# Optimization experiments

Measured on AMD Instinct MI355X. Metric: run time of the kernel, lower is better.

The kernel has to match this reference:

```python
import jax, jax.numpy as jnp
import numpy as np

B, D, O, K = 8192, 256, 256, 16


def setup_inputs() -> dict:
    key = jax.random.key(0)
    k1, k2, k3, k4 = jax.random.split(key, 4)
    x = jax.random.normal(k1, (B, D), dtype=jnp.float32)
    # learned params
    values = jax.random.uniform(k2, (O, D, K), dtype=jnp.float32, minval=-0.05, maxval=0.05)
    skip_w = jax.random.normal(k3, (O, D), dtype=jnp.float32) * (1.0 / np.sqrt(D))
    skip_b = jax.random.uniform(k4, (O,), dtype=jnp.float32, minval=-1.0, maxval=1.0) / np.sqrt(D)
    # fixed buffer (non-trainable)
    grid = jnp.linspace(-1.0, 1.0, K).astype(jnp.float32)
    return {"x": x, "values": values, "skip_w": skip_w, "skip_b": skip_b, "grid": grid}


def reference(x, values, skip_w, skip_b, grid):
    # x: [B, D]; values: [O, D, K]; grid: [K]
    num_knots = grid.shape[0]
    xc = jnp.clip(x, -1.0, 1.0)
    # torch.bucketize(x, grid) (right=False) == searchsorted side='left'
    right = jnp.searchsorted(grid, xc, side="left")            # [B, D]
    left = jnp.clip(right - 1, 0, num_knots - 2)               # [B, D]
    right = left + 1
    g0 = grid[left]
    g1 = grid[right]
    w = (xc - g0) / (g1 - g0 + 1e-12)                          # [B, D]
    # sparse linear-interp coefficients over knots: 2 nonzeros per (b, d)
    coeff = (1.0 - w)[..., None] * jax.nn.one_hot(left, num_knots, dtype=xc.dtype) \
          + w[..., None] * jax.nn.one_hot(right, num_knots, dtype=xc.dtype)  # [B, D, K]
    # y[b,o] = sum_d sum_k coeff[b,d,k] * values[o,d,k]  (== per-dim gather+interp+accumulate)
    y = jnp.einsum("bdk,odk->bo", coeff, values)
    y = y + xc @ skip_w.T + skip_b
    return y
```

## Files before the change

### kernel.cpp

```cpp
#include <hip/hip_runtime.h>
#include <hip/hip_bf16.h>
#include <stdint.h>


#define D_DIM  256
#define O_DIM  256
#define BM     128
#define BK     64
#define KS     4
#define ITERS  16
#define NTHR   512

typedef __attribute__((ext_vector_type(8))) short bf16x8;
typedef __attribute__((ext_vector_type(4))) float f32x4;

__global__ __launch_bounds__(256) void kan_prep(
    const float* __restrict__ values,
    const float* __restrict__ skip_w,
    const float* __restrict__ gknots,
    const float* __restrict__ x,
    unsigned short* __restrict__ Vp)
{
    int tid = blockIdx.x * blockDim.x + threadIdx.x;
    int e = tid * 8;
    int o = e >> 12;
    int kflat = e & 4095;
    float sw = skip_w[(o << 8) | (kflat >> 4)];
    int kmod = kflat & 15;

    const float4* vp4 = reinterpret_cast<const float4*>(values + e);
    float4 v0 = vp4[0], v1 = vp4[1];
    float f[8] = {v0.x, v0.y, v0.z, v0.w, v1.x, v1.y, v1.z, v1.w};
    unsigned int w[4];
#pragma unroll
    for (int j = 0; j < 4; ++j) {
        float2 ab;
        ab.x = f[2*j]     + gknots[kmod + 2*j]     * sw;
        ab.y = f[2*j + 1] + gknots[kmod + 2*j + 1] * sw;
        __hip_bfloat162 p2 = __float22bfloat162_rn(ab);
        __builtin_memcpy(&w[j], &p2, 4);
    }
    size_t c = (size_t)(kflat >> 3) * 256 + (size_t)o;
    *reinterpret_cast<uint4*>(Vp + c * 8) = make_uint4(w[0], w[1], w[2], w[3]);

    {
        int pb = (int)blockIdx.x;
        int mt = (pb & 7) + 8 * ((pb >> 3) & 7);
        int rowbase = mt * BM + (pb >> 6) * 16;
        int t = (int)threadIdx.x;
        const float4* xw = reinterpret_cast<const float4*>(
            x + (size_t)(rowbase + (t >> 4)) * D_DIM) + (t & 15) * 4;
        float s = 0.f;
#pragma unroll
        for (int k = 0; k < 4; ++k) {
            float4 v = xw[k];
            s += v.x + v.y + v.z + v.w;
        }
        asm volatile("" :: "v"(s));
    }
}

__global__ __launch_bounds__(NTHR, 2) void kan_gemm(
    const float* __restrict__ x,
    const unsigned short* __restrict__ Vp,
    float* __restrict__ part,
    float* __restrict__ out)
{
    __shared__ unsigned short As[2][BM * BK];

    const int t    = threadIdx.x;
    const int lane = t & 63;
    const int wid  = t >> 6;
    const int wm   = wid >> 2;
    const int wn   = wid & 3;
    const int l15  = lane & 15;
    const int lhi  = lane >> 4;

    const int bid = (int)blockIdx.x;
    const int m8  = bid & 7;
    const int ks  = (bid >> 3) & 3;
    const int mhi = bid >> 5;
    const int mt  = m8 + 8 * mhi;
    const int bm0 = mt * BM;
    const size_t kc0 = (size_t)ks * 128;

    const int ar = t >> 2;
    const int ad = t & 3;
    const float* xp = x + (size_t)(bm0 + ar) * D_DIM + ks * 64 + ad;

    char* arow[2] = { (char*)&As[0][0] + ar * 128, (char*)&As[1][0] + ar * 128 };
    const int ca = ((2 * ad)     ^ (ar & 7)) * 16;
    const int cb = ((2 * ad + 1) ^ (ar & 7)) * 16;

    auto stageA = [&](int buf, float xv) {
        float xc = fminf(1.f, fmaxf(-1.f, xv));
        float tt = (xc + 1.f) * 7.5f;
        int li = (int)tt;
        li = li > 14 ? 14 : li;
        float w1 = tt - (float)li;
        float2 cw; cw.x = 1.f - w1; cw.y = w1;
        __hip_bfloat162 p2 = __float22bfloat162_rn(cw);
        unsigned int pk;
        __builtin_memcpy(&pk, &p2, 4);
        unsigned long long w64 = (unsigned long long)pk << ((li & 1) * 16);
        unsigned int lo = (unsigned int)w64;
        unsigned int hi = (unsigned int)(w64 >> 32);
        int jl = li >> 1;
        unsigned int wd[8];
#pragma unroll
        for (int j = 0; j < 8; ++j)
            wd[j] = (j == jl) ? lo : ((j == jl + 1) ? hi : 0u);
        char* a = arow[buf];
        *reinterpret_cast<uint4*>(a + ca) = make_uint4(wd[0], wd[1], wd[2], wd[3]);
        *reinterpret_cast<uint4*>(a + cb) = make_uint4(wd[4], wd[5], wd[6], wd[7]);
    };

    #define LOADB(BG, KT)                                                      \
        {                                                                      \
            const unsigned short* _b =                                         \
                Vp + (kc0 + (size_t)(KT) * 8) * 2048;                          \
            _Pragma("unroll")                                                  \
            for (int kh = 0; kh < 2; ++kh)                                     \
                _Pragma("unroll")                                              \
                for (int ni = 0; ni < 4; ++ni) {                               \
                    int n = wn * 64 + ni * 16 + l15;                           \
                    BG[kh * 4 + ni] = *reinterpret_cast<const bf16x8*>(        \
                        _b + ((size_t)((kh * 4 + lhi) * 256 + n)) * 8);        \
                }                                                              \
        }

    f32x4 acc[4][4] = {};
    bf16x8 bgA[8], bgB[8], bgC[8];

    int abyte[4], a7[4];
#pragma unroll
    for (int mi = 0; mi < 4; ++mi) {
        int m = wm * 64 + mi * 16 + l15;
        abyte[mi] = m * 128;
        a7[mi] = m & 7;
    }

    float xnxt = xp[0];
    LOADB(bgA, 0)
    LOADB(bgB, 1)
    stageA(0, xnxt);
    xnxt = xp[4];
    asm volatile("s_waitcnt lgkmcnt(0)" ::: "memory");
    __builtin_amdgcn_s_barrier();
    __builtin_amdgcn_sched_barrier(0);

    #define IT(KT, CUR, BGC_, BGN2)                                            \
        {                                                                      \
            const bool last = (KT) == ITERS - 1;                               \
            if ((KT) + 2 < ITERS) { LOADB(BGN2, (KT) + 2) }                    \
            const char* Ab = (const char*)&As[CUR][0];                         \
            bf16x8 af[4];                                                      \
                                                                   \
            _Pragma("unroll")                                                  \
            for (int mi = 0; mi < 4; ++mi)                                     \
                af[mi] = *reinterpret_cast<const bf16x8*>(                     \
                    Ab + abyte[mi] + ((lhi ^ a7[mi]) << 4));                   \
            __builtin_amdgcn_s_setprio(1);                                     \
            _Pragma("unroll")                                                  \
            for (int mi = 0; mi < 4; ++mi)                                     \
                _Pragma("unroll")                                              \
                for (int ni = 0; ni < 4; ++ni)                                 \
                    acc[mi][ni] = __builtin_amdgcn_mfma_f32_16x16x32_bf16(     \
                        af[mi], BGC_[ni], acc[mi][ni], 0, 0, 0);               \
            __builtin_amdgcn_s_setprio(0);                                     \
                                      \
            if (!last) {                                                       \
                stageA((CUR) ^ 1, xnxt);                                       \
                if ((KT) + 2 < ITERS) xnxt = xp[((KT) + 2) * 4];               \
            }                                                                  \
                                                                   \
            _Pragma("unroll")                                                  \
            for (int mi = 0; mi < 4; ++mi)                                     \
                af[mi] = *reinterpret_cast<const bf16x8*>(                     \
                    Ab + abyte[mi] + (((4 + lhi) ^ a7[mi]) << 4));             \
            __builtin_amdgcn_s_setprio(1);                                     \
            _Pragma("unroll")                                                  \
            for (int mi = 0; mi < 4; ++mi)                                     \
                _Pragma("unroll")                                              \
                for (int ni = 0; ni < 4; ++ni)                                 \
                    acc[mi][ni] = __builtin_amdgcn_mfma_f32_16x16x32_bf16(     \
                        af[mi], BGC_[4 + ni], acc[mi][ni], 0, 0, 0);           \
            __builtin_amdgcn_s_setprio(0);                                     \
            if (!last) {                                                       \
                asm volatile("s_waitcnt lgkmcnt(0)" ::: "memory");             \
                __builtin_amdgcn_s_barrier();                                  \
                __builtin_amdgcn_sched_barrier(0);                             \
            }                                                                  \
        }

    IT(0, 0, bgA, bgC)  IT(1, 1, bgB, bgA)  IT(2, 0, bgC, bgB)
    IT(3, 1, bgA, bgC)  IT(4, 0, bgB, bgA)  IT(5, 1, bgC, bgB)
    IT(6, 0, bgA, bgC)  IT(7, 1, bgB, bgA)  IT(8, 0, bgC, bgB)
    IT(9, 1, bgA, bgC)  IT(10, 0, bgB, bgA) IT(11, 1, bgC, bgB)
    IT(12, 0, bgA, bgC) IT(13, 1, bgB, bgA) IT(14, 0, bgC, bgB)
    IT(15, 1, bgA, bgC)
    #undef IT
    #undef LOADB

    float* dst = (ks == 0) ? out : part + (size_t)(ks - 1) * (8192 * 256);
#pragma unroll
    for (int ni = 0; ni < 4; ++ni) {
        int col = wn * 64 + ni * 16 + l15;
#pragma unroll
        for (int mi = 0; mi < 4; ++mi) {
            f32x4 v = acc[mi][ni];
            int row0 = bm0 + wm * 64 + mi * 16 + lhi * 4;
#pragma unroll
            for (int r = 0; r < 4; ++r)
                dst[(size_t)(row0 + r) * O_DIM + col] = v[r];
        }
    }
}

__global__ __launch_bounds__(256) void kan_reduce(
    const float* __restrict__ part,
    const float* __restrict__ skip_b,
    float* __restrict__ out)
{
    int rbid = (int)blockIdx.x;
    int c    = rbid & 7;
    int tq   = rbid >> 3;
    int mhi  = tq >> 5;
    int sub  = tq & 31;
    int mt   = c + 8 * mhi;
    int row0 = mt * BM + sub * 4;

    int i   = (int)threadIdx.x;
    int row = row0 + (i >> 6);
    int col = (i & 63) * 4;
    size_t e = (size_t)row * O_DIM + col;

    f32x4 s = *reinterpret_cast<const f32x4*>(out + e);
    s += *reinterpret_cast<const f32x4*>(skip_b + col);
    s += *reinterpret_cast<const f32x4*>(part + e);
    s += *reinterpret_cast<const f32x4*>(part + (size_t)8192 * 256 + e);
    s += *reinterpret_cast<const f32x4*>(part + (size_t)2 * 8192 * 256 + e);
    *reinterpret_cast<f32x4*>(out + e) = s;
}

__global__ __launch_bounds__(256) void kan_naive(
    const float* __restrict__ x,
    const unsigned short* __restrict__ Vp,
    const float* __restrict__ skip_b,
    float* __restrict__ out)
{
    int b = blockIdx.x, o = threadIdx.x;
    float acc = skip_b[o];
    for (int d = 0; d < 256; ++d) {
        float xc = fminf(1.f, fmaxf(-1.f, x[(size_t)b * 256 + d]));
        float tt = (xc + 1.f) * 7.5f;
        int li = (int)tt; li = li > 14 ? 14 : li;
        float w1 = tt - (float)li;
        int k0 = d * 16 + li;
        unsigned short u0 = Vp[((size_t)(k0 >> 3) * 256 + o) * 8 + (k0 & 7)];
        int k1 = k0 + 1;
        unsigned short u1 = Vp[((size_t)(k1 >> 3) * 256 + o) * 8 + (k1 & 7)];
        float f0 = __uint_as_float((unsigned)u0 << 16);
        float f1 = __uint_as_float((unsigned)u1 << 16);
        acc += (1.f - w1) * f0 + w1 * f1;
    }
    out[(size_t)b * 256 + o] = acc;
}

extern "C" void kernel_launch(void* const* d_in, const int* in_sizes, int n_in,
                              void* d_out, int out_size, void* d_ws, size_t ws_size,
                              hipStream_t stream) {
    const float* x      = (const float*)d_in[0];
    const float* values = (const float*)d_in[1];
    const float* skip_w = (const float*)d_in[2];
    const float* skip_b = (const float*)d_in[3];
    const float* gknots = (const float*)d_in[4];
    float* out = (float*)d_out;
    (void)in_sizes; (void)n_in; (void)out_size;

    unsigned short* Vp = (unsigned short*)d_ws;
    float* part = (float*)((char*)d_ws + 2u * 1024 * 1024);

    kan_prep<<<dim3(512), dim3(256), 0, stream>>>(values, skip_w, gknots, x, Vp);

    const size_t need = 2u * 1024 * 1024
                      + (size_t)3 * 8192 * 256 * sizeof(float);
    if (ws_size >= need) {
        kan_gemm<<<dim3(256), dim3(NTHR), 0, stream>>>(x, Vp, part, out);
        kan_reduce<<<dim3(2048), dim3(256), 0, stream>>>(part, skip_b, out);
    } else {
        kan_naive<<<dim3(8192), dim3(256), 0, stream>>>(x, Vp, skip_b, out);
    }
}
```

Measured before the change: 40.27 us.

## Give each wave private A tiles to eliminate block barriers in KAN GEMM

Halves the M tile to 64 rows with 256 threads and doubles the grid. Each wave now stages its own copy of the interpolation-coefficient A tile in LDS from float4 x loads, so the per-iteration workgroup barrier can be dropped. The cost is redundant coefficient computation and LDS writes across the four waves, plus more blocks and reloads of the B tiles.

```diff
diff --git a/kernel.cpp b/kernel.cpp
--- a/kernel.cpp
+++ b/kernel.cpp
@@ -5,11 +5,11 @@
 
 #define D_DIM  256
 #define O_DIM  256
-#define BM     128
+#define BM     64
 #define BK     64
 #define KS     4
 #define ITERS  16
-#define NTHR   512
+#define NTHR   256
 
 typedef __attribute__((ext_vector_type(8))) short bf16x8;
 typedef __attribute__((ext_vector_type(4))) float f32x4;
@@ -45,8 +45,8 @@
 
     {
         int pb = (int)blockIdx.x;
-        int mt = (pb & 7) + 8 * ((pb >> 3) & 7);
-        int rowbase = mt * BM + (pb >> 6) * 16;
+        int mt = (pb & 7) + 8 * ((pb >> 3) & 15);
+        int rowbase = mt * BM + (pb >> 7) * 16;
         int t = (int)threadIdx.x;
         const float4* xw = reinterpret_cast<const float4*>(
             x + (size_t)(rowbase + (t >> 4)) * D_DIM) + (t & 15) * 4;
@@ -66,13 +66,11 @@
     float* __restrict__ part,
     float* __restrict__ out)
 {
-    __shared__ unsigned short As[2][BM * BK];
+    __shared__ unsigned short As[4][2][64 * 64];
 
     const int t    = threadIdx.x;
     const int lane = t & 63;
     const int wid  = t >> 6;
-    const int wm   = wid >> 2;
-    const int wn   = wid & 3;
     const int l15  = lane & 15;
     const int lhi  = lane >> 4;
 
@@ -84,35 +82,39 @@
     const int bm0 = mt * BM;
     const size_t kc0 = (size_t)ks * 128;
 
-    const int ar = t >> 2;
-    const int ad = t & 3;
-    const float* xp = x + (size_t)(bm0 + ar) * D_DIM + ks * 64 + ad;
-
-    char* arow[2] = { (char*)&As[0][0] + ar * 128, (char*)&As[1][0] + ar * 128 };
-    const int ca = ((2 * ad)     ^ (ar & 7)) * 16;
-    const int cb = ((2 * ad + 1) ^ (ar & 7)) * 16;
-
-    auto stageA = [&](int buf, float xv) {
-        float xc = fminf(1.f, fmaxf(-1.f, xv));
-        float tt = (xc + 1.f) * 7.5f;
-        int li = (int)tt;
-        li = li > 14 ? 14 : li;
-        float w1 = tt - (float)li;
-        float2 cw; cw.x = 1.f - w1; cw.y = w1;
-        __hip_bfloat162 p2 = __float22bfloat162_rn(cw);
-        unsigned int pk;
-        __builtin_memcpy(&pk, &p2, 4);
-        unsigned long long w64 = (unsigned long long)pk << ((li & 1) * 16);
-        unsigned int lo = (unsigned int)w64;
-        unsigned int hi = (unsigned int)(w64 >> 32);
-        int jl = li >> 1;
-        unsigned int wd[8];
-#pragma unroll
-        for (int j = 0; j < 8; ++j)
-            wd[j] = (j == jl) ? lo : ((j == jl + 1) ? hi : 0u);
-        char* a = arow[buf];
-        *reinterpret_cast<uint4*>(a + ca) = make_uint4(wd[0], wd[1], wd[2], wd[3]);
-        *reinterpret_cast<uint4*>(a + cb) = make_uint4(wd[4], wd[5], wd[6], wd[7]);
+    const float* xr = x + (size_t)(bm0 + lane) * D_DIM + ks * 64;
+
+    char* abase[2] = { (char*)&As[wid][0][0] + lane * 128,
+                       (char*)&As[wid][1][0] + lane * 128 };
+    const int lsw = lane & 7;
+
+    auto stageA = [&](int buf, float4 xv) {
+        float vv[4] = {xv.x, xv.y, xv.z, xv.w};
+        char* base = abase[buf];
+#pragma unroll
+        for (int d = 0; d < 4; ++d) {
+            float xc = fminf(1.f, fmaxf(-1.f, vv[d]));
+            float tt = (xc + 1.f) * 7.5f;
+            int li = (int)tt;
+            li = li > 14 ? 14 : li;
+            float w1 = tt - (float)li;
+            float2 cw; cw.x = 1.f - w1; cw.y = w1;
+            __hip_bfloat162 p2 = __float22bfloat162_rn(cw);
+            unsigned int pk;
+            __builtin_memcpy(&pk, &p2, 4);
+            unsigned long long w64 = (unsigned long long)pk << ((li & 1) * 16);
+            unsigned int lo = (unsigned int)w64;
+            unsigned int hi = (unsigned int)(w64 >> 32);
+            int jl = li >> 1;
+            unsigned int wd[8];
+#pragma unroll
+            for (int j = 0; j < 8; ++j)
+                wd[j] = (j == jl) ? lo : ((j == jl + 1) ? hi : 0u);
+            *reinterpret_cast<uint4*>(base + (((2 * d)     ^ lsw) << 4)) =
+                make_uint4(wd[0], wd[1], wd[2], wd[3]);
+            *reinterpret_cast<uint4*>(base + (((2 * d + 1) ^ lsw) << 4)) =
+                make_uint4(wd[4], wd[5], wd[6], wd[7]);
+        }
     };
 
     #define LOADB(BG, KT)                                                      \
@@ -123,7 +125,7 @@
             for (int kh = 0; kh < 2; ++kh)                                     \
                 _Pragma("unroll")                                              \
                 for (int ni = 0; ni < 4; ++ni) {                               \
-                    int n = wn * 64 + ni * 16 + l15;                           \
+                    int n = wid * 64 + ni * 16 + l15;                          \
                     BG[kh * 4 + ni] = *reinterpret_cast<const bf16x8*>(        \
                         _b + ((size_t)((kh * 4 + lhi) * 256 + n)) * 8);        \
                 }                                                              \
@@ -132,34 +134,28 @@
     f32x4 acc[4][4] = {};
     bf16x8 bgA[8], bgB[8], bgC[8];
 
-    int abyte[4], a7[4];
-#pragma unroll
-    for (int mi = 0; mi < 4; ++mi) {
-        int m = wm * 64 + mi * 16 + l15;
-        abyte[mi] = m * 128;
-        a7[mi] = m & 7;
-    }
-
-    float xnxt = xp[0];
+    int abyte[4];
+#pragma unroll
+    for (int mi = 0; mi < 4; ++mi) abyte[mi] = (mi * 16 + l15) * 128;
+    const int a7 = l15 & 7;
+
+    float4 xcur = *reinterpret_cast<const float4*>(xr);
     LOADB(bgA, 0)
     LOADB(bgB, 1)
-    stageA(0, xnxt);
-    xnxt = xp[4];
-    asm volatile("s_waitcnt lgkmcnt(0)" ::: "memory");
-    __builtin_amdgcn_s_barrier();
-    __builtin_amdgcn_sched_barrier(0);
+    stageA(0, xcur);
+    float4 xn = *reinterpret_cast<const float4*>(xr + 4);
 
     #define IT(KT, CUR, BGC_, BGN2)                                            \
         {                                                                      \
             const bool last = (KT) == ITERS - 1;                               \
             if ((KT) + 2 < ITERS) { LOADB(BGN2, (KT) + 2) }                    \
-            const char* Ab = (const char*)&As[CUR][0];                         \
+            const char* Ab = (const char*)&As[wid][CUR][0];                    \
             bf16x8 af[4];                                                      \
                                                                    \
             _Pragma("unroll")                                                  \
             for (int mi = 0; mi < 4; ++mi)                                     \
                 af[mi] = *reinterpret_cast<const bf16x8*>(                     \
-                    Ab + abyte[mi] + ((lhi ^ a7[mi]) << 4));                   \
+                    Ab + abyte[mi] + ((lhi ^ a7) << 4));                       \
             __builtin_amdgcn_s_setprio(1);                                     \
             _Pragma("unroll")                                                  \
             for (int mi = 0; mi < 4; ++mi)                                     \
@@ -168,16 +164,17 @@
                     acc[mi][ni] = __builtin_amdgcn_mfma_f32_16x16x32_bf16(     \
                         af[mi], BGC_[ni], acc[mi][ni], 0, 0, 0);               \
             __builtin_amdgcn_s_setprio(0);                                     \
-                                      \
+                                    \
             if (!last) {                                                       \
-                stageA((CUR) ^ 1, xnxt);                                       \
-                if ((KT) + 2 < ITERS) xnxt = xp[((KT) + 2) * 4];               \
+                stageA((CUR) ^ 1, xn);                                         \
+                if ((KT) + 2 < ITERS)                                          \
+                    xn = *reinterpret_cast<const float4*>(xr + ((KT) + 2) * 4);\
             }                                                                  \
                                                                    \
             _Pragma("unroll")                                                  \
             for (int mi = 0; mi < 4; ++mi)                                     \
                 af[mi] = *reinterpret_cast<const bf16x8*>(                     \
-                    Ab + abyte[mi] + (((4 + lhi) ^ a7[mi]) << 4));             \
+                    Ab + abyte[mi] + (((4 + lhi) ^ a7) << 4));                 \
             __builtin_amdgcn_s_setprio(1);                                     \
             _Pragma("unroll")                                                  \
             for (int mi = 0; mi < 4; ++mi)                                     \
@@ -186,11 +183,6 @@
                     acc[mi][ni] = __builtin_amdgcn_mfma_f32_16x16x32_bf16(     \
                         af[mi], BGC_[4 + ni], acc[mi][ni], 0, 0, 0);           \
             __builtin_amdgcn_s_setprio(0);                                     \
-            if (!last) {                                                       \
-                asm volatile("s_waitcnt lgkmcnt(0)" ::: "memory");             \
-                __builtin_amdgcn_s_barrier();                                  \
-                __builtin_amdgcn_sched_barrier(0);                             \
-            }                                                                  \
         }
 
     IT(0, 0, bgA, bgC)  IT(1, 1, bgB, bgA)  IT(2, 0, bgC, bgB)
@@ -205,11 +197,11 @@
     float* dst = (ks == 0) ? out : part + (size_t)(ks - 1) * (8192 * 256);
 #pragma unroll
     for (int ni = 0; ni < 4; ++ni) {
-        int col = wn * 64 + ni * 16 + l15;
+        int col = wid * 64 + ni * 16 + l15;
 #pragma unroll
         for (int mi = 0; mi < 4; ++mi) {
             f32x4 v = acc[mi][ni];
-            int row0 = bm0 + wm * 64 + mi * 16 + lhi * 4;
+            int row0 = bm0 + mi * 16 + lhi * 4;
 #pragma unroll
             for (int r = 0; r < 4; ++r)
                 dst[(size_t)(row0 + r) * O_DIM + col] = v[r];
@@ -225,8 +217,8 @@
     int rbid = (int)blockIdx.x;
     int c    = rbid & 7;
     int tq   = rbid >> 3;
-    int mhi  = tq >> 5;
-    int sub  = tq & 31;
+    int mhi  = tq >> 4;
+    int sub  = tq & 15;
     int mt   = c + 8 * mhi;
     int row0 = mt * BM + sub * 4;
 
@@ -286,7 +278,7 @@
     const size_t need = 2u * 1024 * 1024
                       + (size_t)3 * 8192 * 256 * sizeof(float);
     if (ws_size >= need) {
-        kan_gemm<<<dim3(256), dim3(NTHR), 0, stream>>>(x, Vp, part, out);
+        kan_gemm<<<dim3(512), dim3(NTHR), 0, stream>>>(x, Vp, part, out);
         kan_reduce<<<dim3(2048), dim3(256), 0, stream>>>(part, skip_b, out);
     } else {
         kan_naive<<<dim3(8192), dim3(256), 0, stream>>>(x, Vp, skip_b, out);
```

Result: slower. 42.13 us (+4.6%).
